# Kernel tuning notes

Hardware: AMD Instinct MI355X
Metric: run time of the kernel (lower is better)

The kernel has to match this reference:

```python
import jax, jax.numpy as jnp
import numpy as np

B, C_IN, T, D, K = 16, 256, 8192, 64, 512


def setup_inputs() -> dict:
    key = jax.random.key(0)
    k1, k2, k3, k4 = jax.random.split(key, 4)
    x = jax.random.normal(k1, (B, C_IN, T), dtype=jnp.float32)
    # 1x1 Conv1d weight [n_out, n_in] (kernel size 1 squeezed) + bias
    W = jax.random.normal(k2, (D, C_IN), dtype=jnp.float32) * (1.0 / np.sqrt(C_IN))
    b = jax.random.normal(k3, (D,), dtype=jnp.float32) * 0.01
    codebook = jax.random.normal(k4, (K, D), dtype=jnp.float32)
    return {"x": x, "W": W, "b": b, "codebook": codebook}


def reference(x, W, b, codebook):
    # 1x1 conv projection: [B, C_IN, T] -> z_e [B, T, D]
    z_e = jnp.einsum('bct,dc->btd', x, W) + b
    # squared L2 distances to all K prototypes: ||z||^2 - 2 z.e + ||e||^2  -> [B, T, K]
    d2 = ((z_e * z_e).sum(-1, keepdims=True)
          - 2.0 * jnp.einsum('btd,kd->btk', z_e, codebook)
          + (codebook * codebook).sum(-1))
    idx = jnp.argmin(d2, axis=-1)          # [B, T] nearest prototype ids
    z_q = codebook[idx]                    # [B, T, D] gathered codebook vectors
    sg = jax.lax.stop_gradient
    # vq_norms[:,:,0] = ||sg(z_e) - e_q||^2  (codebook/vq loss term)
    # vq_norms[:,:,1] = ||z_e - sg(e_q)||^2  (commitment loss term)
    n0 = ((sg(z_e) - z_q) ** 2).sum(-1)
    n1 = ((z_e - sg(z_q)) ** 2).sum(-1)
    return jnp.stack([n0, n1], axis=-1)    # [B, T, 2]
```

## Files before the change

### kernel.cpp

```cpp
#include <hip/hip_runtime.h>

#define B_   16
#define CIN  256
#define T_   8192
#define D_   64
#define KK   512

typedef __attribute__((ext_vector_type(8)))  short short8v;
typedef __attribute__((ext_vector_type(16))) float f32x16;

__device__ __forceinline__ unsigned f2bf(float f) {
    union { float f; unsigned u; } v; v.f = f;
    unsigned r = v.u + 0x7fffu + ((v.u >> 16) & 1u);
    return r >> 16;
}

__global__ __launch_bounds__(512, 2) void fused_kernel(
    const float* __restrict__ x, const float* __restrict__ W,
    const float* __restrict__ bias, const float* __restrict__ cb,
    float* __restrict__ out)
{
    __shared__ char smem[134400];
    unsigned short* cbb = (unsigned short*)smem;
    unsigned short* Wl  = (unsigned short*)(smem + 65536);
    unsigned short* xsb = (unsigned short*)(smem + 98304);
    unsigned short* zl  = (unsigned short*)(smem + 98304);
    float* n2b = (float*)(smem + 131072);
    float* znb = (float*)(smem + 133120);
    float* bl  = (float*)(smem + 134144);

    const int tid  = threadIdx.x;
    const int bid  = blockIdx.x;
    const int b    = bid >> 5;
    const int t0   = (bid & 31) << 8;
    const int lane = tid & 63;
    const int l31  = lane & 31;
    const int lh   = lane >> 5;
    const int wid  = tid >> 6;

    const float* xb = x + (size_t)(b * CIN) * T_ + t0;

    {
        const float* cr = cb + (size_t)tid * 64;
        float s = 0.f;
        #pragma unroll
        for (int sl = 0; sl < 8; ++sl) {
            float4 a4 = *(const float4*)(cr + sl * 8);
            float4 b4 = *(const float4*)(cr + sl * 8 + 4);
            s = fmaf(a4.x, a4.x, s); s = fmaf(a4.y, a4.y, s);
            s = fmaf(a4.z, a4.z, s); s = fmaf(a4.w, a4.w, s);
            s = fmaf(b4.x, b4.x, s); s = fmaf(b4.y, b4.y, s);
            s = fmaf(b4.z, b4.z, s); s = fmaf(b4.w, b4.w, s);
            uint4 pk;
            pk.x = f2bf(a4.x) | (f2bf(a4.y) << 16);
            pk.y = f2bf(a4.z) | (f2bf(a4.w) << 16);
            pk.z = f2bf(b4.x) | (f2bf(b4.y) << 16);
            pk.w = f2bf(b4.z) | (f2bf(b4.w) << 16);
            ((uint4*)cbb)[tid * 8 + (sl ^ (tid & 7))] = pk;
        }
        n2b[tid] = s;
        if (tid < 64) bl[tid] = bias[tid];
    }

    {
        const int d  = tid >> 3;
        const int c0 = (tid & 7) * 32;
        const float* wr = W + (size_t)d * CIN + c0;
        #pragma unroll
        for (int q = 0; q < 4; ++q) {
            float4 a4 = *(const float4*)(wr + q * 8);
            float4 b4 = *(const float4*)(wr + q * 8 + 4);
            uint4 pk;
            pk.x = f2bf(a4.x) | (f2bf(a4.y) << 16);
            pk.y = f2bf(a4.z) | (f2bf(a4.w) << 16);
            pk.z = f2bf(b4.x) | (f2bf(b4.y) << 16);
            pk.w = f2bf(b4.z) | (f2bf(b4.w) << 16);
            const int s = (c0 >> 3) + q;
            ((uint4*)Wl)[d * 32 + (s ^ (d & 7))] = pk;
        }
    }

#define LOADX(dst, ch_) do {                                                  \
        _Pragma("unroll")                                                     \
        for (int p = 0; p < 4; ++p) {                                         \
            int id_ = p * 512 + tid;                                          \
            int cl_ = id_ >> 6;                                               \
            int tl_ = (id_ & 63) << 2;                                        \
            dst[p] = *(const float4*)(xb + (size_t)((ch_) * 32 + cl_) * T_ + tl_); \
        }                                                                     \
    } while (0)

#define WRITEX(src, bsel_) do {                                               \
        _Pragma("unroll")                                                     \
        for (int p = 0; p < 4; ++p) {                                         \
            int id_ = p * 512 + tid;                                          \
            int cl_ = id_ >> 6;                                               \
            int tl_ = (id_ & 63) << 2;                                        \
            uint2 pk_;                                                        \
            pk_.x = f2bf(src[p].x) | (f2bf(src[p].y) << 16);                  \
            pk_.y = f2bf(src[p].z) | (f2bf(src[p].w) << 16);                  \
            *(uint2*)(xsb + (bsel_) * 8192 + (cl_ << 8) + tl_) = pk_;         \
        }                                                                     \
    } while (0)

    float4 st[4];
    LOADX(st, 0);
    WRITEX(st, 0);
    __syncthreads();

    const int dtile = wid >> 2;
    const int tt0   = (wid & 3) * 2;

    f32x16 acc0 = (f32x16)(0.0f), acc1 = (f32x16)(0.0f);

    #pragma unroll 1
    for (int ch = 0; ch < 8; ++ch) {
        if (ch + 1 < 8) LOADX(st, ch + 1);
        const unsigned short* xr = xsb + (ch & 1) * 8192;
        #pragma unroll
        for (int k2 = 0; k2 < 2; ++k2) {
            const int d = dtile * 32 + l31;
            const int s = (ch * 2 + k2) * 2 + lh;
            uint4 wv = ((const uint4*)Wl)[d * 32 + (s ^ (d & 7))];
            short8v wa = __builtin_bit_cast(short8v, wv);
            #pragma unroll
            for (int q = 0; q < 2; ++q) {
                const int t  = (tt0 + q) * 32 + l31;
                const unsigned short* xp = xr + (k2 * 16 + lh * 8) * 256 + t;
                unsigned r0 = xp[0],    r1 = xp[256],  r2 = xp[512],  r3 = xp[768];
                unsigned r4 = xp[1024], r5 = xp[1280], r6 = xp[1536], r7 = xp[1792];
                uint4 bv;
                bv.x = r0 | (r1 << 16); bv.y = r2 | (r3 << 16);
                bv.z = r4 | (r5 << 16); bv.w = r6 | (r7 << 16);
                short8v xa = __builtin_bit_cast(short8v, bv);
                if (q == 0)
                    acc0 = __builtin_amdgcn_mfma_f32_32x32x16_bf16(wa, xa, acc0, 0, 0, 0);
                else
                    acc1 = __builtin_amdgcn_mfma_f32_32x32x16_bf16(wa, xa, acc1, 0, 0, 0);
            }
        }
        __syncthreads();
        if (ch + 1 < 8) WRITEX(st, (ch + 1) & 1);
        __syncthreads();
    }

    float zsum[2];
    #pragma unroll
    for (int q = 0; q < 2; ++q) {
        f32x16& A = q ? acc1 : acc0;
        const int t = (tt0 + q) * 32 + l31;
        float ss = 0.f;
        #pragma unroll
        for (int r = 0; r < 16; ++r) {
            const int d = dtile * 32 + (r & 3) + 8 * (r >> 2) + 4 * lh;
            float v = A[r] + bl[d];
            A[r] = v;
            ss = fmaf(v, v, ss);
        }
        ss += __shfl_xor(ss, 32);
        zsum[q] = ss;
        #pragma unroll
        for (int g = 0; g < 4; ++g) {
            const int dq = dtile * 32 + 8 * g + 4 * lh;
            uint2 pk;
            pk.x = f2bf(A[4 * g + 0]) | (f2bf(A[4 * g + 1]) << 16);
            pk.y = f2bf(A[4 * g + 2]) | (f2bf(A[4 * g + 3]) << 16);
            const int s    = dq >> 3;
            const int half = (dq >> 2) & 1;
            *(uint2*)((char*)zl + t * 128 + ((s ^ (t & 7)) << 4) + (half << 3)) = pk;
        }
    }
    if (dtile == 0 && lh == 0) {
        znb[(tt0 + 0) * 32 + l31] = zsum[0];
        znb[(tt0 + 1) * 32 + l31] = zsum[1];
    }
    __syncthreads();
    if (dtile == 1 && lh == 0) {
        znb[(tt0 + 0) * 32 + l31] += zsum[0];
        znb[(tt0 + 1) * 32 + l31] += zsum[1];
    }
    __syncthreads();

    const int tt = wid;
    short8v az[4];
    #pragma unroll
    for (int ks = 0; ks < 4; ++ks) {
        const int t = tt * 32 + l31;
        const int s = ks * 2 + lh;
        uint4 v = *(const uint4*)((char*)zl + t * 128 + ((s ^ (t & 7)) << 4));
        az[ks] = __builtin_bit_cast(short8v, v);
    }

    float rmin[16];
    #pragma unroll
    for (int r = 0; r < 16; ++r) rmin[r] = 3.0e38f;

    #pragma unroll 1
    for (int nt = 0; nt < 16; ++nt) {
        const int n = nt * 32 + l31;
        const float n2v = n2b[n];
        short8v bfr[4];
        #pragma unroll
        for (int ks = 0; ks < 4; ++ks) {
            const int s = ks * 2 + lh;
            uint4 v = ((const uint4*)cbb)[n * 8 + (s ^ (n & 7))];
            bfr[ks] = __builtin_bit_cast(short8v, v);
        }
        f32x16 acc = (f32x16)(0.0f);
        acc = __builtin_amdgcn_mfma_f32_32x32x16_bf16(az[0], bfr[0], acc, 0, 0, 0);
        acc = __builtin_amdgcn_mfma_f32_32x32x16_bf16(az[1], bfr[1], acc, 0, 0, 0);
        acc = __builtin_amdgcn_mfma_f32_32x32x16_bf16(az[2], bfr[2], acc, 0, 0, 0);
        acc = __builtin_amdgcn_mfma_f32_32x32x16_bf16(az[3], bfr[3], acc, 0, 0, 0);
        #pragma unroll
        for (int r = 0; r < 16; ++r)
            rmin[r] = fminf(rmin[r], fmaf(-2.f, acc[r], n2v));
    }

    #pragma unroll
    for (int m = 1; m <= 16; m <<= 1) {
        #pragma unroll
        for (int r = 0; r < 16; ++r)
            rmin[r] = fminf(rmin[r], __shfl_xor(rmin[r], m));
    }

    if (l31 == 0) {
        #pragma unroll
        for (int r = 0; r < 16; ++r) {
            const int t = tt * 32 + (r & 3) + 8 * (r >> 2) + 4 * lh;
            float v = znb[t] + rmin[r];
            float2 o; o.x = v; o.y = v;
            *(float2*)(out + (size_t)((bid << 8) + t) * 2) = o;
        }
    }
#undef LOADX
#undef WRITEX
}

extern "C" void kernel_launch(void* const* d_in, const int* in_sizes, int n_in,
                              void* d_out, int out_size, void* d_ws, size_t ws_size,
                              hipStream_t stream) {
    const float* x    = (const float*)d_in[0];
    const float* W    = (const float*)d_in[1];
    const float* bias = (const float*)d_in[2];
    const float* cb   = (const float*)d_in[3];
    float* out = (float*)d_out;
    (void)d_ws; (void)ws_size;

    fused_kernel<<<512, 512, 0, stream>>>(x, W, bias, cb, out);
}
```

Before: 218.6 us.

## Precompute bf16 weights/codebook in prep kernel and stream x directly from global

A small prep kernel converts W and the codebook to bf16 in a workspace buffer and computes the codebook norms once, so the per-block conversion of those tensors is removed. The fused kernel drops to 256 threads with a much smaller LDS footprint to allow more blocks per CU. It loads x straight from global memory into MFMA operands, with no LDS double buffering and no barriers in the projection loop. Codebook fragments are likewise read from global/L2 instead of LDS. The trade-off is strided scalar global loads of x (one float per channel row) and repeated global codebook reads per wave, in exchange for less setup work and higher occupancy.

```diff
diff --git a/kernel.cpp b/kernel.cpp
--- a/kernel.cpp
+++ b/kernel.cpp
@@ -1,4 +1,5 @@
 #include <hip/hip_runtime.h>
+#include <hip/hip_bf16.h>
 
 #define B_   16
 #define CIN  256
@@ -8,26 +9,46 @@
 
 typedef __attribute__((ext_vector_type(8)))  short short8v;
 typedef __attribute__((ext_vector_type(16))) float f32x16;
+typedef unsigned short ushort_t;
 
 __device__ __forceinline__ unsigned f2bf(float f) {
     union { float f; unsigned u; } v; v.f = f;
     unsigned r = v.u + 0x7fffu + ((v.u >> 16) & 1u);
     return r >> 16;
 }
-
-__global__ __launch_bounds__(512, 2) void fused_kernel(
-    const float* __restrict__ x, const float* __restrict__ W,
-    const float* __restrict__ bias, const float* __restrict__ cb,
-    float* __restrict__ out)
+__device__ __forceinline__ unsigned pk2(float lo, float hi) {
+    union { __hip_bfloat162 h; unsigned u; } v;
+    v.h = __float22bfloat162_rn(make_float2(lo, hi));
+    return v.u;
+}
+
+__global__ __launch_bounds__(256) void prep_kernel(
+    const float* __restrict__ W, const float* __restrict__ cb,
+    ushort_t* __restrict__ W16, ushort_t* __restrict__ cb16,
+    float* __restrict__ n2)
 {
-    __shared__ char smem[134400];
-    unsigned short* cbb = (unsigned short*)smem;
-    unsigned short* Wl  = (unsigned short*)(smem + 65536);
-    unsigned short* xsb = (unsigned short*)(smem + 98304);
-    unsigned short* zl  = (unsigned short*)(smem + 98304);
-    float* n2b = (float*)(smem + 131072);
-    float* znb = (float*)(smem + 133120);
-    float* bl  = (float*)(smem + 134144);
+    const int i = blockIdx.x * 256 + threadIdx.x;
+    W16[i] = (ushort_t)f2bf(W[i]);
+    cb16[i]         = (ushort_t)f2bf(cb[i]);
+    cb16[i + 16384] = (ushort_t)f2bf(cb[i + 16384]);
+    if (i < KK) {
+        const float* cr = cb + (size_t)i * 64;
+        float s = 0.f;
+        #pragma unroll
+        for (int d = 0; d < 64; ++d) s = fmaf(cr[d], cr[d], s);
+        n2[i] = s;
+    }
+}
+
+__global__ __launch_bounds__(256, 3) void fused_kernel(
+    const float* __restrict__ x, const ushort_t* __restrict__ W16,
+    const float* __restrict__ bias, const ushort_t* __restrict__ cb16,
+    const float* __restrict__ n2g, float* __restrict__ out)
+{
+    __shared__ ushort_t zl[256 * 64];
+    __shared__ float n2b[512];
+    __shared__ float znb[256];
+    __shared__ float bl[64];
 
     const int tid  = threadIdx.x;
     const int bid  = blockIdx.x;
@@ -38,202 +59,138 @@
     const int lh   = lane >> 5;
     const int wid  = tid >> 6;
 
-    const float* xb = x + (size_t)(b * CIN) * T_ + t0;
-
-    {
-        const float* cr = cb + (size_t)tid * 64;
-        float s = 0.f;
-        #pragma unroll
-        for (int sl = 0; sl < 8; ++sl) {
-            float4 a4 = *(const float4*)(cr + sl * 8);
-            float4 b4 = *(const float4*)(cr + sl * 8 + 4);
-            s = fmaf(a4.x, a4.x, s); s = fmaf(a4.y, a4.y, s);
-            s = fmaf(a4.z, a4.z, s); s = fmaf(a4.w, a4.w, s);
-            s = fmaf(b4.x, b4.x, s); s = fmaf(b4.y, b4.y, s);
-            s = fmaf(b4.z, b4.z, s); s = fmaf(b4.w, b4.w, s);
-            uint4 pk;
-            pk.x = f2bf(a4.x) | (f2bf(a4.y) << 16);
-            pk.y = f2bf(a4.z) | (f2bf(a4.w) << 16);
-            pk.z = f2bf(b4.x) | (f2bf(b4.y) << 16);
-            pk.w = f2bf(b4.z) | (f2bf(b4.w) << 16);
-            ((uint4*)cbb)[tid * 8 + (sl ^ (tid & 7))] = pk;
-        }
-        n2b[tid] = s;
-        if (tid < 64) bl[tid] = bias[tid];
-    }
-
-    {
-        const int d  = tid >> 3;
-        const int c0 = (tid & 7) * 32;
-        const float* wr = W + (size_t)d * CIN + c0;
-        #pragma unroll
-        for (int q = 0; q < 4; ++q) {
-            float4 a4 = *(const float4*)(wr + q * 8);
-            float4 b4 = *(const float4*)(wr + q * 8 + 4);
-            uint4 pk;
-            pk.x = f2bf(a4.x) | (f2bf(a4.y) << 16);
-            pk.y = f2bf(a4.z) | (f2bf(a4.w) << 16);
-            pk.z = f2bf(b4.x) | (f2bf(b4.y) << 16);
-            pk.w = f2bf(b4.z) | (f2bf(b4.w) << 16);
-            const int s = (c0 >> 3) + q;
-            ((uint4*)Wl)[d * 32 + (s ^ (d & 7))] = pk;
-        }
-    }
-
-#define LOADX(dst, ch_) do {                                                  \
+    n2b[tid]       = n2g[tid];
+    n2b[tid + 256] = n2g[tid + 256];
+    if (tid < 64) bl[tid] = bias[tid];
+    __syncthreads();
+
+    const int twav = wid << 6;
+    const ushort_t* wp = W16 + l31 * CIN + lh * 8;
+    const float* xB = x + (size_t)(b * CIN + lh * 8) * T_ + t0 + twav + l31;
+
+    f32x16 a00 = (f32x16)(0.f), a01 = (f32x16)(0.f);
+    f32x16 a10 = (f32x16)(0.f), a11 = (f32x16)(0.f);
+
+    #pragma unroll 2
+    for (int kk = 0; kk < 16; ++kk) {
+        uint4 w0 = *(const uint4*)(wp + kk * 16);
+        uint4 w1 = *(const uint4*)(wp + 8192 + kk * 16);
+        short8v wa0 = __builtin_bit_cast(short8v, w0);
+        short8v wa1 = __builtin_bit_cast(short8v, w1);
+        const float* xk = xB + (size_t)(kk * 16) * T_;
+        #pragma unroll
+        for (int q = 0; q < 2; ++q) {
+            const float* xp = xk + q * 32;
+            float f0 = xp[0];
+            float f1 = xp[(size_t)1 * T_];
+            float f2 = xp[(size_t)2 * T_];
+            float f3 = xp[(size_t)3 * T_];
+            float f4 = xp[(size_t)4 * T_];
+            float f5 = xp[(size_t)5 * T_];
+            float f6 = xp[(size_t)6 * T_];
+            float f7 = xp[(size_t)7 * T_];
+            uint4 bv;
+            bv.x = pk2(f0, f1); bv.y = pk2(f2, f3);
+            bv.z = pk2(f4, f5); bv.w = pk2(f6, f7);
+            short8v xa = __builtin_bit_cast(short8v, bv);
+            if (q == 0) {
+                a00 = __builtin_amdgcn_mfma_f32_32x32x16_bf16(wa0, xa, a00, 0, 0, 0);
+                a10 = __builtin_amdgcn_mfma_f32_32x32x16_bf16(wa1, xa, a10, 0, 0, 0);
+            } else {
+                a01 = __builtin_amdgcn_mfma_f32_32x32x16_bf16(wa0, xa, a01, 0, 0, 0);
+                a11 = __builtin_amdgcn_mfma_f32_32x32x16_bf16(wa1, xa, a11, 0, 0, 0);
+            }
+        }
+    }
+
+    float zs0 = 0.f, zs1 = 0.f;
+#define EPI(A, dt_, q_, zs_) do {                                             \
+        const int t_ = twav + (q_) * 32 + l31;                                \
+        float ss_ = 0.f;                                                      \
         _Pragma("unroll")                                                     \
-        for (int p = 0; p < 4; ++p) {                                         \
-            int id_ = p * 512 + tid;                                          \
-            int cl_ = id_ >> 6;                                               \
-            int tl_ = (id_ & 63) << 2;                                        \
-            dst[p] = *(const float4*)(xb + (size_t)((ch_) * 32 + cl_) * T_ + tl_); \
+        for (int r = 0; r < 16; ++r) {                                        \
+            const int d_ = (dt_) * 32 + (r & 3) + 8 * (r >> 2) + 4 * lh;      \
+            float v_ = A[r] + bl[d_];                                         \
+            A[r] = v_;                                                        \
+            ss_ = fmaf(v_, v_, ss_);                                          \
+        }                                                                     \
+        zs_ += ss_;                                                           \
+        _Pragma("unroll")                                                     \
+        for (int g = 0; g < 4; ++g) {                                         \
+            const int dq_ = (dt_) * 32 + 8 * g + 4 * lh;                      \
+            uint2 pk_;                                                        \
+            pk_.x = pk2(A[4 * g + 0], A[4 * g + 1]);                          \
+            pk_.y = pk2(A[4 * g + 2], A[4 * g + 3]);                          \
+            const int s_    = dq_ >> 3;                                       \
+            const int half_ = (dq_ >> 2) & 1;                                 \
+            *(uint2*)((char*)zl + t_ * 128 + ((s_ ^ (t_ & 7)) << 4)           \
+                      + (half_ << 3)) = pk_;                                  \
         }                                                                     \
     } while (0)
 
-#define WRITEX(src, bsel_) do {                                               \
-        _Pragma("unroll")                                                     \
-        for (int p = 0; p < 4; ++p) {                                         \
-            int id_ = p * 512 + tid;                                          \
-            int cl_ = id_ >> 6;                                               \
-            int tl_ = (id_ & 63) << 2;                                        \
-            uint2 pk_;                                                        \
-            pk_.x = f2bf(src[p].x) | (f2bf(src[p].y) << 16);                  \
-            pk_.y = f2bf(src[p].z) | (f2bf(src[p].w) << 16);                  \
-            *(uint2*)(xsb + (bsel_) * 8192 + (cl_ << 8) + tl_) = pk_;         \
-        }                                                                     \
-    } while (0)
-
-    float4 st[4];
-    LOADX(st, 0);
-    WRITEX(st, 0);
+    EPI(a00, 0, 0, zs0);
+    EPI(a01, 0, 1, zs1);
+    EPI(a10, 1, 0, zs0);
+    EPI(a11, 1, 1, zs1);
+#undef EPI
+    zs0 += __shfl_xor(zs0, 32);
+    zs1 += __shfl_xor(zs1, 32);
+    if (lh == 0) {
+        znb[twav + l31]      = zs0;
+        znb[twav + 32 + l31] = zs1;
+    }
     __syncthreads();
 
-    const int dtile = wid >> 2;
-    const int tt0   = (wid & 3) * 2;
-
-    f32x16 acc0 = (f32x16)(0.0f), acc1 = (f32x16)(0.0f);
-
     #pragma unroll 1
-    for (int ch = 0; ch < 8; ++ch) {
-        if (ch + 1 < 8) LOADX(st, ch + 1);
-        const unsigned short* xr = xsb + (ch & 1) * 8192;
-        #pragma unroll
-        for (int k2 = 0; k2 < 2; ++k2) {
-            const int d = dtile * 32 + l31;
-            const int s = (ch * 2 + k2) * 2 + lh;
-            uint4 wv = ((const uint4*)Wl)[d * 32 + (s ^ (d & 7))];
-            short8v wa = __builtin_bit_cast(short8v, wv);
-            #pragma unroll
-            for (int q = 0; q < 2; ++q) {
-                const int t  = (tt0 + q) * 32 + l31;
-                const unsigned short* xp = xr + (k2 * 16 + lh * 8) * 256 + t;
-                unsigned r0 = xp[0],    r1 = xp[256],  r2 = xp[512],  r3 = xp[768];
-                unsigned r4 = xp[1024], r5 = xp[1280], r6 = xp[1536], r7 = xp[1792];
-                uint4 bv;
-                bv.x = r0 | (r1 << 16); bv.y = r2 | (r3 << 16);
-                bv.z = r4 | (r5 << 16); bv.w = r6 | (r7 << 16);
-                short8v xa = __builtin_bit_cast(short8v, bv);
-                if (q == 0)
-                    acc0 = __builtin_amdgcn_mfma_f32_32x32x16_bf16(wa, xa, acc0, 0, 0, 0);
-                else
-                    acc1 = __builtin_amdgcn_mfma_f32_32x32x16_bf16(wa, xa, acc1, 0, 0, 0);
-            }
-        }
-        __syncthreads();
-        if (ch + 1 < 8) WRITEX(st, (ch + 1) & 1);
-        __syncthreads();
-    }
-
-    float zsum[2];
-    #pragma unroll
-    for (int q = 0; q < 2; ++q) {
-        f32x16& A = q ? acc1 : acc0;
-        const int t = (tt0 + q) * 32 + l31;
-        float ss = 0.f;
-        #pragma unroll
-        for (int r = 0; r < 16; ++r) {
-            const int d = dtile * 32 + (r & 3) + 8 * (r >> 2) + 4 * lh;
-            float v = A[r] + bl[d];
-            A[r] = v;
-            ss = fmaf(v, v, ss);
-        }
-        ss += __shfl_xor(ss, 32);
-        zsum[q] = ss;
-        #pragma unroll
-        for (int g = 0; g < 4; ++g) {
-            const int dq = dtile * 32 + 8 * g + 4 * lh;
-            uint2 pk;
-            pk.x = f2bf(A[4 * g + 0]) | (f2bf(A[4 * g + 1]) << 16);
-            pk.y = f2bf(A[4 * g + 2]) | (f2bf(A[4 * g + 3]) << 16);
-            const int s    = dq >> 3;
-            const int half = (dq >> 2) & 1;
-            *(uint2*)((char*)zl + t * 128 + ((s ^ (t & 7)) << 4) + (half << 3)) = pk;
-        }
-    }
-    if (dtile == 0 && lh == 0) {
-        znb[(tt0 + 0) * 32 + l31] = zsum[0];
-        znb[(tt0 + 1) * 32 + l31] = zsum[1];
-    }
-    __syncthreads();
-    if (dtile == 1 && lh == 0) {
-        znb[(tt0 + 0) * 32 + l31] += zsum[0];
-        znb[(tt0 + 1) * 32 + l31] += zsum[1];
-    }
-    __syncthreads();
-
-    const int tt = wid;
-    short8v az[4];
-    #pragma unroll
-    for (int ks = 0; ks < 4; ++ks) {
-        const int t = tt * 32 + l31;
-        const int s = ks * 2 + lh;
-        uint4 v = *(const uint4*)((char*)zl + t * 128 + ((s ^ (t & 7)) << 4));
-        az[ks] = __builtin_bit_cast(short8v, v);
-    }
-
-    float rmin[16];
-    #pragma unroll
-    for (int r = 0; r < 16; ++r) rmin[r] = 3.0e38f;
-
-    #pragma unroll 1
-    for (int nt = 0; nt < 16; ++nt) {
-        const int n = nt * 32 + l31;
-        const float n2v = n2b[n];
-        short8v bfr[4];
+    for (int tl = 0; tl < 2; ++tl) {
+        const int tt = wid * 2 + tl;
+        const int t  = tt * 32 + l31;
+        short8v az[4];
         #pragma unroll
         for (int ks = 0; ks < 4; ++ks) {
             const int s = ks * 2 + lh;
-            uint4 v = ((const uint4*)cbb)[n * 8 + (s ^ (n & 7))];
-            bfr[ks] = __builtin_bit_cast(short8v, v);
-        }
-        f32x16 acc = (f32x16)(0.0f);
-        acc = __builtin_amdgcn_mfma_f32_32x32x16_bf16(az[0], bfr[0], acc, 0, 0, 0);
-        acc = __builtin_amdgcn_mfma_f32_32x32x16_bf16(az[1], bfr[1], acc, 0, 0, 0);
-        acc = __builtin_amdgcn_mfma_f32_32x32x16_bf16(az[2], bfr[2], acc, 0, 0, 0);
-        acc = __builtin_amdgcn_mfma_f32_32x32x16_bf16(az[3], bfr[3], acc, 0, 0, 0);
-        #pragma unroll
-        for (int r = 0; r < 16; ++r)
-            rmin[r] = fminf(rmin[r], fmaf(-2.f, acc[r], n2v));
-    }
-
-    #pragma unroll
-    for (int m = 1; m <= 16; m <<= 1) {
-        #pragma unroll
-        for (int r = 0; r < 16; ++r)
-            rmin[r] = fminf(rmin[r], __shfl_xor(rmin[r], m));
-    }
-
-    if (l31 == 0) {
-        #pragma unroll
-        for (int r = 0; r < 16; ++r) {
-            const int t = tt * 32 + (r & 3) + 8 * (r >> 2) + 4 * lh;
-            float v = znb[t] + rmin[r];
-            float2 o; o.x = v; o.y = v;
-            *(float2*)(out + (size_t)((bid << 8) + t) * 2) = o;
-        }
-    }
-#undef LOADX
-#undef WRITEX
+            uint4 v = *(const uint4*)((char*)zl + t * 128 + ((s ^ (t & 7)) << 4));
+            az[ks] = __builtin_bit_cast(short8v, v);
+        }
+        float rmin[16];
+        #pragma unroll
+        for (int r = 0; r < 16; ++r) rmin[r] = 3.0e38f;
+
+        const ushort_t* cbp = cb16 + l31 * 64 + lh * 8;
+        #pragma unroll 1
+        for (int nt = 0; nt < 16; ++nt) {
+            const int n = nt * 32 + l31;
+            const float n2v = n2b[n];
+            const ushort_t* cq = cbp + nt * 2048;
+            uint4 v0 = *(const uint4*)(cq);
+            uint4 v1 = *(const uint4*)(cq + 16);
+            uint4 v2 = *(const uint4*)(cq + 32);
+            uint4 v3 = *(const uint4*)(cq + 48);
+            f32x16 acc = (f32x16)(0.f);
+            acc = __builtin_amdgcn_mfma_f32_32x32x16_bf16(az[0], __builtin_bit_cast(short8v, v0), acc, 0, 0, 0);
+            acc = __builtin_amdgcn_mfma_f32_32x32x16_bf16(az[1], __builtin_bit_cast(short8v, v1), acc, 0, 0, 0);
+            acc = __builtin_amdgcn_mfma_f32_32x32x16_bf16(az[2], __builtin_bit_cast(short8v, v2), acc, 0, 0, 0);
+            acc = __builtin_amdgcn_mfma_f32_32x32x16_bf16(az[3], __builtin_bit_cast(short8v, v3), acc, 0, 0, 0);
+            #pragma unroll
+            for (int r = 0; r < 16; ++r)
+                rmin[r] = fminf(rmin[r], fmaf(-2.f, acc[r], n2v));
+        }
+        #pragma unroll
+        for (int m = 1; m <= 16; m <<= 1) {
+            #pragma unroll
+            for (int r = 0; r < 16; ++r)
+                rmin[r] = fminf(rmin[r], __shfl_xor(rmin[r], m));
+        }
+        if (l31 == 0) {
+            #pragma unroll
+            for (int r = 0; r < 16; ++r) {
+                const int tr = tt * 32 + (r & 3) + 8 * (r >> 2) + 4 * lh;
+                float v = znb[tr] + rmin[r];
+                float2 o; o.x = v; o.y = v;
+                *(float2*)(out + (size_t)((bid << 8) + tr) * 2) = o;
+            }
+        }
+    }
 }
 
 extern "C" void kernel_launch(void* const* d_in, const int* in_sizes, int n_in,
@@ -244,7 +201,11 @@
     const float* bias = (const float*)d_in[2];
     const float* cb   = (const float*)d_in[3];
     float* out = (float*)d_out;
-    (void)d_ws; (void)ws_size;
-
-    fused_kernel<<<512, 512, 0, stream>>>(x, W, bias, cb, out);
-}
+
+    ushort_t* W16  = (ushort_t*)d_ws;
+    ushort_t* cb16 = W16 + 16384;
+    float*    n2   = (float*)(cb16 + 32768);
+
+    prep_kernel<<<64, 256, 0, stream>>>(W, cb, W16, cb16, n2);
+    fused_kernel<<<512, 256, 0, stream>>>(x, W16, bias, cb16, n2, out);
+}
```

Measured after the change: 267.4 us. 1.22x slower.
